# Optimization experiments

Measured on AMD Instinct MI355X. Metric: run time of the kernel, lower is better.

## Reference

```python
import jax, jax.numpy as jnp
import numpy as np

B = 16384          # graphs per batch
NUM_NODES = 32     # nodes per graph
EMBED = 64         # embed_dim (GCNConv in=out, conv1mult=1)
DEG = 8            # avg in-graph degree
OUT = 2            # outputSize
N = B * NUM_NODES
E = N * DEG
HID = NUM_NODES * EMBED  # size_in1 = size_out1 = 2048


def setup_inputs() -> dict:
    key = jax.random.key(0)
    ks = jax.random.split(key, 10)
    x = jax.random.normal(ks[0], (N, EMBED), dtype=jnp.float32)
    # edges constrained within each graph of NUM_NODES nodes
    offs = jnp.repeat(jnp.arange(B, dtype=jnp.int64) * NUM_NODES, DEG * NUM_NODES)
    src = jax.random.randint(ks[1], (E,), 0, NUM_NODES, dtype=jnp.int64) + offs
    dst = jax.random.randint(ks[2], (E,), 0, NUM_NODES, dtype=jnp.int64) + offs
    edge_index = jnp.stack([src, dst], axis=0)
    batch = jnp.repeat(jnp.arange(B, dtype=jnp.int64), NUM_NODES)
    s = 0.05
    Wc = jax.random.normal(ks[3], (EMBED, EMBED), dtype=jnp.float32) * s
    bc = jnp.zeros((EMBED,), dtype=jnp.float32)
    W1 = jax.random.normal(ks[4], (HID, HID), dtype=jnp.float32) * (1.0 / np.sqrt(HID))
    b1 = jnp.zeros((HID,), dtype=jnp.float32)
    W2 = jax.random.normal(ks[5], (OUT, HID), dtype=jnp.float32) * (1.0 / np.sqrt(HID))
    b2 = jnp.zeros((OUT,), dtype=jnp.float32)
    return {"x": x, "Wc": Wc, "bc": bc, "W1": W1, "b1": b1,
            "W2": W2, "b2": b2, "edge_index": edge_index, "batch": batch}


def gcn_conv(x, Wc, bc, edge_index):
    # PyG GCNConv: linear transform, add self-loops, symmetric normalization,
    # scatter-add aggregation at target nodes, then bias.
    n = x.shape[0]
    h = x @ Wc.T                                        # [N, F]
    loop = jnp.arange(n, dtype=edge_index.dtype)
    row = jnp.concatenate([edge_index[0], loop])        # sources
    col = jnp.concatenate([edge_index[1], loop])        # targets
    deg = jax.ops.segment_sum(jnp.ones_like(col, dtype=h.dtype), col,
                              num_segments=n)           # in-degree incl. self-loop
    dinv = jnp.where(deg > 0, jax.lax.rsqrt(deg), 0.0)
    norm = dinv[row] * dinv[col]                        # [E+N]
    msgs = h[row] * norm[:, None]                       # gather + scale
    out = jax.ops.segment_sum(msgs, col, num_segments=n)  # scatter-add
    return out + bc


def reference(x, Wc, bc, W1, b1, W2, b2, edge_index, batch):
    h = gcn_conv(x, Wc, bc, edge_index)
    h = jax.nn.relu(h)
    h = h.reshape(B, HID)                # [B, numNodes*embed_dim]
    h = h @ W1.T + b1                    # lin1 (dropout is eval-mode identity)
    h = jax.nn.relu(h)
    h = h @ W2.T + b2                    # lin2
    return jax.nn.softmax(h, axis=-1)    # [B, OUT]
```

## Files before the change

kernel.cpp:

```cpp
#include <hip/hip_runtime.h>

#define NGRAPH 16384
#define NNODE  32
#define EMB    64
#define HIDDIM 2048
#define ETOT   4194304
#define EPG    256

typedef __attribute__((ext_vector_type(8))) short bf16x8_t;
typedef __attribute__((ext_vector_type(8))) unsigned short u16x8_t;
typedef __attribute__((ext_vector_type(4))) float f32x4_t;

__device__ __forceinline__ unsigned short f2bf(float v) {
  unsigned int u = __float_as_uint(v);
  u += 0x7fffu + ((u >> 16) & 1u);
  return (unsigned short)(u >> 16);
}
__device__ __forceinline__ float bf2f(unsigned short u) {
  return __uint_as_float(((unsigned int)u) << 16);
}
__device__ __forceinline__ unsigned int cvtpk(float lo, float hi) {
  unsigned int r;
  asm("v_cvt_pk_bf16_f32 %0, %1, %2" : "=v"(r) : "v"(lo), "v"(hi));
  return r;
}
__device__ __forceinline__ bf16x8_t pack8(float4 a, float4 b) {
  union { unsigned int u[4]; bf16x8_t v; } r;
  r.u[0] = cvtpk(a.x, a.y); r.u[1] = cvtpk(a.z, a.w);
  r.u[2] = cvtpk(b.x, b.y); r.u[3] = cvtpk(b.z, b.w);
  return r.v;
}

#define GLDS(SRC, DST)                                                          \
  __builtin_amdgcn_global_load_lds(                                             \
      (const __attribute__((address_space(1))) void*)(SRC),                     \
      (__attribute__((address_space(3))) void*)(DST), 16, 0, 0)

__global__ __launch_bounds__(256, 4) void front_kernel(const float* __restrict__ x,
                                                       const float* __restrict__ Wc,
                                                       const float* __restrict__ bc,
                                                       const int* __restrict__ ei,
                                                       unsigned short* __restrict__ abf,
                                                       const float* __restrict__ W1,
                                                       unsigned short* __restrict__ W1b) {
  __shared__ __align__(16) char smem[40960];

  if (blockIdx.x >= 4096) {
    float* row = (float*)smem;
    const int r = blockIdx.x - 4096, t = threadIdx.x;
    const float4* p = (const float4*)(W1 + (size_t)r * HIDDIM);
    *(float4*)&row[t * 8]     = p[t * 2];
    *(float4*)&row[t * 8 + 4] = p[t * 2 + 1];
    __syncthreads();
    const int feat = t >> 2, nb = (t & 3) * 8;
    u16x8_t o;
    #pragma unroll
    for (int j = 0; j < 8; ++j) o[j] = f2bf(row[(nb + j) * 64 + feat]);
    *(u16x8_t*)(W1b + (size_t)r * HIDDIM + t * 8) = o;
    return;
  }

  const int wv = threadIdx.x >> 6, lane = threadIdx.x & 63;
  const int g = blockIdx.x * 4 + wv;
  char* my = smem + wv * 10240;
  unsigned int*   adjcnt = (unsigned int*)my;
  unsigned short* adjb   = (unsigned short*)my;
  unsigned short* outT   = (unsigned short*)my;
  unsigned short* hT     = (unsigned short*)(my + 5120);
  const int lr = lane & 15, lk = lane >> 4;

  const float* xg = x + (size_t)g * (NNODE * EMB);
  float4 xr[2][2][2];
  #pragma unroll
  for (int mt = 0; mt < 2; ++mt)
    #pragma unroll
    for (int kk = 0; kk < 2; ++kk) {
      const float* p = xg + (mt * 16 + lr) * EMB + kk * 32 + lk * 8;
      xr[mt][kk][0] = *(const float4*)p;
      xr[mt][kk][1] = *(const float4*)(p + 4);
    }

  int sl[4], dl[4];
  #pragma unroll
  for (int j = 0; j < 4; ++j) {
    sl[j] = ei[(size_t)g * EPG + j * 64 + lane] - g * NNODE;
    dl[j] = ei[(size_t)ETOT + (size_t)g * EPG + j * 64 + lane] - g * NNODE;
  }

  {
    uint4 z = {0u, 0u, 0u, 0u};
    #pragma unroll
    for (int i = 0; i < 4; ++i) *(uint4*)&adjcnt[lane * 16 + i * 4] = z;
  }
  asm volatile("" ::: "memory");
  #pragma unroll
  for (int j = 0; j < 4; ++j) atomicAdd(&adjcnt[dl[j] * 32 + sl[j]], 1u);
  asm volatile("" ::: "memory");

  const int rr = lane >> 1, hh = lane & 1;
  uint4 c[4];
  unsigned int cs = 0;
  #pragma unroll
  for (int i = 0; i < 4; ++i) {
    c[i] = *(const uint4*)&adjcnt[rr * 32 + hh * 16 + i * 4];
    cs += c[i].x + c[i].y + c[i].z + c[i].w;
  }
  cs += (unsigned int)__shfl_xor((int)cs, 1);
  const float dinvr = rsqrtf(1.0f + (float)cs);
  asm volatile("" ::: "memory");
  {
    float vals[16];
    #pragma unroll
    for (int i = 0; i < 4; ++i) {
      const unsigned int cc[4] = {c[i].x, c[i].y, c[i].z, c[i].w};
      #pragma unroll
      for (int e = 0; e < 4; ++e) {
        const int s = hh * 16 + i * 4 + e;
        const float ds = __shfl(dinvr, s * 2);
        const float cnt = (float)cc[e] + ((s == rr) ? 1.0f : 0.0f);
        vals[i * 4 + e] = cnt * dinvr * ds;
      }
    }
    union { unsigned int u[8]; u16x8_t v[2]; } pk;
    #pragma unroll
    for (int i = 0; i < 8; ++i) pk.u[i] = cvtpk(vals[2 * i], vals[2 * i + 1]);
    *(u16x8_t*)&adjb[rr * 40 + hh * 16]     = pk.v[0];
    *(u16x8_t*)&adjb[rr * 40 + hh * 16 + 8] = pk.v[1];
  }

  bf16x8_t xa[2][2];
  #pragma unroll
  for (int mt = 0; mt < 2; ++mt)
    #pragma unroll
    for (int kk = 0; kk < 2; ++kk) xa[mt][kk] = pack8(xr[mt][kk][0], xr[mt][kk][1]);
  f32x4_t hc[2][4];
  #pragma unroll
  for (int mt = 0; mt < 2; ++mt)
    #pragma unroll
    for (int nt = 0; nt < 4; ++nt) hc[mt][nt] = (f32x4_t){0.f, 0.f, 0.f, 0.f};
  #pragma unroll
  for (int nt = 0; nt < 4; ++nt)
    #pragma unroll
    for (int kk = 0; kk < 2; ++kk) {
      const float* p = Wc + (nt * 16 + lr) * EMB + kk * 32 + lk * 8;
      const bf16x8_t wb = pack8(*(const float4*)p, *(const float4*)(p + 4));
      #pragma unroll
      for (int mt = 0; mt < 2; ++mt)
        hc[mt][nt] = __builtin_amdgcn_mfma_f32_16x16x32_bf16(xa[mt][kk], wb, hc[mt][nt], 0, 0, 0);
    }
  #pragma unroll
  for (int mt = 0; mt < 2; ++mt)
    #pragma unroll
    for (int nt = 0; nt < 4; ++nt) {
      uint2 pk;
      pk.x = cvtpk(hc[mt][nt][0], hc[mt][nt][1]);
      pk.y = cvtpk(hc[mt][nt][2], hc[mt][nt][3]);
      *(uint2*)&hT[(nt * 16 + lr) * 40 + mt * 16 + lk * 4] = pk;
    }
  asm volatile("" ::: "memory");

  bf16x8_t aj[2];
  #pragma unroll
  for (int mt = 0; mt < 2; ++mt)
    aj[mt] = *(const bf16x8_t*)&adjb[(mt * 16 + lr) * 40 + lk * 8];
  f32x4_t oc[2][4];
  #pragma unroll
  for (int mt = 0; mt < 2; ++mt)
    #pragma unroll
    for (int nt = 0; nt < 4; ++nt) oc[mt][nt] = (f32x4_t){0.f, 0.f, 0.f, 0.f};
  #pragma unroll
  for (int nt = 0; nt < 4; ++nt) {
    const bf16x8_t hb = *(const bf16x8_t*)&hT[(nt * 16 + lr) * 40 + lk * 8];
    #pragma unroll
    for (int mt = 0; mt < 2; ++mt)
      oc[mt][nt] = __builtin_amdgcn_mfma_f32_16x16x32_bf16(aj[mt], hb, oc[mt][nt], 0, 0, 0);
  }
  asm volatile("" ::: "memory");

  #pragma unroll
  for (int nt = 0; nt < 4; ++nt) {
    const float bcv = bc[nt * 16 + lr];
    #pragma unroll
    for (int mt = 0; mt < 2; ++mt) {
      float v0 = fmaxf(oc[mt][nt][0] + bcv, 0.0f);
      float v1 = fmaxf(oc[mt][nt][1] + bcv, 0.0f);
      float v2 = fmaxf(oc[mt][nt][2] + bcv, 0.0f);
      float v3 = fmaxf(oc[mt][nt][3] + bcv, 0.0f);
      uint2 pk;
      pk.x = cvtpk(v0, v1);
      pk.y = cvtpk(v2, v3);
      *(uint2*)&outT[(nt * 16 + lr) * 40 + mt * 16 + lk * 4] = pk;
    }
  }
  asm volatile("" ::: "memory");

  unsigned short* og = abf + (size_t)g * HIDDIM;
  #pragma unroll
  for (int j = 0; j < 4; ++j) {
    const int e = lane * 8 + j * 512;
    const int feat = e >> 5, nb = e & 31;
    *(u16x8_t*)(og + e) = *(const u16x8_t*)&outT[feat * 40 + nb];
  }
}

__global__ __launch_bounds__(512, 1) void lin1_kernel(const unsigned short* __restrict__ A,
                                                      const unsigned short* __restrict__ Bw,
                                                      const float* __restrict__ b1,
                                                      const float* __restrict__ W2,
                                                      float2* __restrict__ part) {
  __shared__ __align__(16) unsigned short sh[65536];

  const int bid = blockIdx.x;
  const int xcd = bid & 7;
  const int g = bid >> 3;
  const int bm = xcd * 8 + (g >> 3);
  const int bn = g & 7;

  const int tid = threadIdx.x;
  const int lane = tid & 63, w = tid >> 6;
  const int wm = w >> 2, wn = w & 3;
  const int lr = lane & 15, lk = lane >> 4;

  const int r0 = tid >> 3;
  const int kge = ((((tid & 7) * 16) ^ ((r0 & 7) << 4)) >> 1);
  const unsigned short* gA = A  + (size_t)(bm * 256 + r0) * HIDDIM + kge;
  const unsigned short* gB = Bw + (size_t)(bn * 256 + r0) * HIDDIM + kge;

  auto stage = [&](const unsigned short* gb, int d, int mat, int half, int tile) {
    const unsigned short* s = gb + (size_t)(half * 128) * HIDDIM + tile * 64;
    unsigned short* l = &sh[d * 32768 + mat * 16384 + half * 8192 + tid * 8];
    GLDS(s, l);
    GLDS(s + (size_t)64 * HIDDIM, l + 4096);
  };

  const int arow = wm * 8192 + lr * 64;
  const int brow = 16384 + (wn >> 1) * 8192 + ((wn & 1) * 64 + lr) * 64;
  int eoff[2];
  eoff[0] = (lk * 8) ^ ((lr & 7) << 3);
  eoff[1] = (32 + lk * 8) ^ ((lr & 7) << 3);

  f32x4_t acc[8][4];
  #pragma unroll
  for (int i = 0; i < 8; ++i)
    #pragma unroll
    for (int j = 0; j < 4; ++j) acc[i][j] = (f32x4_t){0.f, 0.f, 0.f, 0.f};

  stage(gA, 0, 0, 0, 0); stage(gA, 0, 0, 1, 0);
  stage(gB, 0, 1, 0, 0); stage(gB, 0, 1, 1, 0);
  stage(gB, 1, 1, 0, 1); stage(gB, 1, 1, 1, 1);
  asm volatile("s_waitcnt vmcnt(4)" ::: "memory");
  __builtin_amdgcn_sched_barrier(0);
  __builtin_amdgcn_s_barrier();

  bf16x8_t af[4][2], bv0[2][2], bv1[2][2];

  for (int it = 0; it < 16; ++it) {
    const int o = 2 * it + 1;
    const bool more = (it < 15);

    #pragma unroll
    for (int half = 0; half < 2; ++half) {
      const int dof = half * 32768;

      #pragma unroll
      for (int mi = 0; mi < 4; ++mi) {
        af[mi][0] = *(const bf16x8_t*)&sh[dof + arow + mi * 1024 + eoff[0]];
        af[mi][1] = *(const bf16x8_t*)&sh[dof + arow + mi * 1024 + eoff[1]];
      }
      #pragma unroll
      for (int ni = 0; ni < 2; ++ni) {
        bv0[ni][0] = *(const bf16x8_t*)&sh[dof + brow + ni * 1024 + eoff[0]];
        bv0[ni][1] = *(const bf16x8_t*)&sh[dof + brow + ni * 1024 + eoff[1]];
        bv1[ni][0] = *(const bf16x8_t*)&sh[dof + brow + (ni + 2) * 1024 + eoff[0]];
        bv1[ni][1] = *(const bf16x8_t*)&sh[dof + brow + (ni + 2) * 1024 + eoff[1]];
      }
      if (half == 0)      { stage(gA, 1, 0, 0, o);     stage(gA, 1, 0, 1, o); }
      else if (more)      { stage(gA, 0, 0, 0, o + 1); stage(gA, 0, 0, 1, o + 1); }
      asm volatile("s_waitcnt lgkmcnt(0)" ::: "memory");
      __builtin_amdgcn_sched_barrier(0);
      __builtin_amdgcn_s_barrier();
      __builtin_amdgcn_s_setprio(1);
      #pragma unroll
      for (int kk = 0; kk < 2; ++kk)
        #pragma unroll
        for (int mi = 0; mi < 4; ++mi)
          #pragma unroll
          for (int ni = 0; ni < 2; ++ni) {
            acc[mi][ni]     = __builtin_amdgcn_mfma_f32_16x16x32_bf16(af[mi][kk], bv0[ni][kk], acc[mi][ni], 0, 0, 0);
            acc[mi][ni + 2] = __builtin_amdgcn_mfma_f32_16x16x32_bf16(af[mi][kk], bv1[ni][kk], acc[mi][ni + 2], 0, 0, 0);
          }
      __builtin_amdgcn_s_setprio(0);

      #pragma unroll
      for (int mi = 0; mi < 4; ++mi) {
        af[mi][0] = *(const bf16x8_t*)&sh[dof + arow + (mi + 4) * 1024 + eoff[0]];
        af[mi][1] = *(const bf16x8_t*)&sh[dof + arow + (mi + 4) * 1024 + eoff[1]];
      }
      if (more) {
        const int tgt = (half == 0) ? (o + 1) : (o + 2);
        stage(gB, half, 1, 0, tgt);
        stage(gB, half, 1, 1, tgt);
      }
      asm volatile("s_waitcnt lgkmcnt(0)" ::: "memory");
      if (more) { asm volatile("s_waitcnt vmcnt(4)" ::: "memory"); }
      else      { asm volatile("s_waitcnt vmcnt(0)" ::: "memory"); }
      __builtin_amdgcn_sched_barrier(0);
      __builtin_amdgcn_s_barrier();
      __builtin_amdgcn_s_setprio(1);
      #pragma unroll
      for (int kk = 0; kk < 2; ++kk)
        #pragma unroll
        for (int mi = 0; mi < 4; ++mi)
          #pragma unroll
          for (int ni = 0; ni < 2; ++ni) {
            acc[mi + 4][ni]     = __builtin_amdgcn_mfma_f32_16x16x32_bf16(af[mi][kk], bv0[ni][kk], acc[mi + 4][ni], 0, 0, 0);
            acc[mi + 4][ni + 2] = __builtin_amdgcn_mfma_f32_16x16x32_bf16(af[mi][kk], bv1[ni][kk], acc[mi + 4][ni + 2], 0, 0, 0);
          }
      __builtin_amdgcn_s_setprio(0);
    }
  }

  const int ccol0 = bn * 256 + wn * 64 + lr;
  float b1v[4], w2a[4], w2b[4];
  #pragma unroll
  for (int ni = 0; ni < 4; ++ni) {
    b1v[ni] = b1[ccol0 + ni * 16];
    w2a[ni] = W2[ccol0 + ni * 16];
    w2b[ni] = W2[HIDDIM + ccol0 + ni * 16];
  }
  float2* pl = (float2*)sh;
  #pragma unroll
  for (int mi = 0; mi < 8; ++mi)
    #pragma unroll
    for (int r = 0; r < 4; ++r) {
      float s0 = 0.0f, s1 = 0.0f;
      #pragma unroll
      for (int ni = 0; ni < 4; ++ni) {
        const float v = fmaxf(acc[mi][ni][r] + b1v[ni], 0.0f);
        s0 = fmaf(v, w2a[ni], s0);
        s1 = fmaf(v, w2b[ni], s1);
      }
      #pragma unroll
      for (int off = 1; off < 16; off <<= 1) {
        s0 += __shfl_xor(s0, off);
        s1 += __shfl_xor(s1, off);
      }
      if (lr == 0) {
        const int rowLocal = wm * 128 + mi * 16 + lk * 4 + r;
        float2 v2; v2.x = s0; v2.y = s1;
        pl[rowLocal * 4 + wn] = v2;
      }
    }
  __syncthreads();
  if (tid < 256) {
    const float2 p0 = pl[tid * 4 + 0];
    const float2 p1 = pl[tid * 4 + 1];
    const float2 p2 = pl[tid * 4 + 2];
    const float2 p3 = pl[tid * 4 + 3];
    float2 o;
    o.x = (p0.x + p1.x) + (p2.x + p3.x);
    o.y = (p0.y + p1.y) + (p2.y + p3.y);
    part[(size_t)bn * NGRAPH + bm * 256 + tid] = o;
  }
}

__global__ __launch_bounds__(256) void softmax_kernel(const float2* __restrict__ part,
                                                      const float* __restrict__ b2,
                                                      float* __restrict__ out) {
  const int i = blockIdx.x * 256 + threadIdx.x;
  float s0 = 0.0f, s1 = 0.0f;
  #pragma unroll
  for (int bn = 0; bn < 8; ++bn) {
    const float2 p = part[(size_t)bn * NGRAPH + i];
    s0 += p.x; s1 += p.y;
  }
  const float l0 = s0 + b2[0];
  const float l1 = s1 + b2[1];
  const float mx = fmaxf(l0, l1);
  const float e0 = expf(l0 - mx);
  const float e1 = expf(l1 - mx);
  const float inv = 1.0f / (e0 + e1);
  float2 o;
  o.x = e0 * inv;
  o.y = e1 * inv;
  *((float2*)out + i) = o;
}

extern "C" void kernel_launch(void* const* d_in, const int* in_sizes, int n_in,
                              void* d_out, int out_size, void* d_ws, size_t ws_size,
                              hipStream_t stream) {
  const float* x  = (const float*)d_in[0];
  const float* Wc = (const float*)d_in[1];
  const float* bc = (const float*)d_in[2];
  const float* W1 = (const float*)d_in[3];
  const float* b1 = (const float*)d_in[4];
  const float* W2 = (const float*)d_in[5];
  const float* b2 = (const float*)d_in[6];
  const int* ei   = (const int*)d_in[7];

  unsigned short* Abf  = (unsigned short*)d_ws;
  unsigned short* W1bf = (unsigned short*)((char*)d_ws + (size_t)67108864);
  float2*         part = (float2*)((char*)d_ws + (size_t)75497472);

  front_kernel<<<dim3(6144), dim3(256), 0, stream>>>(x, Wc, bc, ei, Abf, W1, W1bf);
  lin1_kernel<<<dim3(512), dim3(512), 0, stream>>>(Abf, W1bf, b1, W2, part);
  softmax_kernel<<<dim3(64), dim3(256), 0, stream>>>(part, b2, (float*)d_out);
}
```

Baseline: 166.0 us.

## Restructure lin1 GEMM pipeline to one barrier per K-tile with triple-buffered B

```diff
diff --git a/kernel.cpp b/kernel.cpp
--- a/kernel.cpp
+++ b/kernel.cpp
@@ -208,7 +208,7 @@
                                                       const float* __restrict__ b1,
                                                       const float* __restrict__ W2,
                                                       float2* __restrict__ part) {
-  __shared__ __align__(16) unsigned short sh[65536];
+  __shared__ __align__(16) unsigned short sh[81920];
 
   const int bid = blockIdx.x;
   const int xcd = bid & 7;
@@ -226,15 +226,21 @@
   const unsigned short* gA = A  + (size_t)(bm * 256 + r0) * HIDDIM + kge;
   const unsigned short* gB = Bw + (size_t)(bn * 256 + r0) * HIDDIM + kge;
 
-  auto stage = [&](const unsigned short* gb, int d, int mat, int half, int tile) {
-    const unsigned short* s = gb + (size_t)(half * 128) * HIDDIM + tile * 64;
-    unsigned short* l = &sh[d * 32768 + mat * 16384 + half * 8192 + tid * 8];
+  auto stageA = [&](int d, int half, int tile) {
+    const unsigned short* s = gA + (size_t)(half * 128) * HIDDIM + tile * 64;
+    unsigned short* l = &sh[d * 16384 + half * 8192 + tid * 8];
     GLDS(s, l);
     GLDS(s + (size_t)64 * HIDDIM, l + 4096);
   };
+  auto stageB = [&](int cb, int half, int tile) {
+    const unsigned short* s = gB + (size_t)(half * 128) * HIDDIM + tile * 64;
+    unsigned short* l = &sh[32768 + cb * 16384 + half * 8192 + tid * 8];
+    GLDS(s, l);
+    GLDS(s + (size_t)64 * HIDDIM, l + 4096);
+  };
 
   const int arow = wm * 8192 + lr * 64;
-  const int brow = 16384 + (wn >> 1) * 8192 + ((wn & 1) * 64 + lr) * 64;
+  const int brow = (wn >> 1) * 8192 + ((wn & 1) * 64 + lr) * 64;
   int eoff[2];
   eoff[0] = (lk * 8) ^ ((lr & 7) << 3);
   eoff[1] = (32 + lk * 8) ^ ((lr & 7) << 3);
@@ -245,79 +251,58 @@
     #pragma unroll
     for (int j = 0; j < 4; ++j) acc[i][j] = (f32x4_t){0.f, 0.f, 0.f, 0.f};
 
-  stage(gA, 0, 0, 0, 0); stage(gA, 0, 0, 1, 0);
-  stage(gB, 0, 1, 0, 0); stage(gB, 0, 1, 1, 0);
-  stage(gB, 1, 1, 0, 1); stage(gB, 1, 1, 1, 1);
+  stageA(0, 0, 0); stageA(0, 1, 0);
+  stageB(0, 0, 0); stageB(0, 1, 0);
+  stageB(1, 0, 1); stageB(1, 1, 1);
   asm volatile("s_waitcnt vmcnt(4)" ::: "memory");
   __builtin_amdgcn_sched_barrier(0);
   __builtin_amdgcn_s_barrier();
 
-  bf16x8_t af[4][2], bv0[2][2], bv1[2][2];
-
-  for (int it = 0; it < 16; ++it) {
-    const int o = 2 * it + 1;
-    const bool more = (it < 15);
-
-    #pragma unroll
-    for (int half = 0; half < 2; ++half) {
-      const int dof = half * 32768;
-
-      #pragma unroll
-      for (int mi = 0; mi < 4; ++mi) {
-        af[mi][0] = *(const bf16x8_t*)&sh[dof + arow + mi * 1024 + eoff[0]];
-        af[mi][1] = *(const bf16x8_t*)&sh[dof + arow + mi * 1024 + eoff[1]];
-      }
-      #pragma unroll
-      for (int ni = 0; ni < 2; ++ni) {
-        bv0[ni][0] = *(const bf16x8_t*)&sh[dof + brow + ni * 1024 + eoff[0]];
-        bv0[ni][1] = *(const bf16x8_t*)&sh[dof + brow + ni * 1024 + eoff[1]];
-        bv1[ni][0] = *(const bf16x8_t*)&sh[dof + brow + (ni + 2) * 1024 + eoff[0]];
-        bv1[ni][1] = *(const bf16x8_t*)&sh[dof + brow + (ni + 2) * 1024 + eoff[1]];
-      }
-      if (half == 0)      { stage(gA, 1, 0, 0, o);     stage(gA, 1, 0, 1, o); }
-      else if (more)      { stage(gA, 0, 0, 0, o + 1); stage(gA, 0, 0, 1, o + 1); }
-      asm volatile("s_waitcnt lgkmcnt(0)" ::: "memory");
-      __builtin_amdgcn_sched_barrier(0);
-      __builtin_amdgcn_s_barrier();
-      __builtin_amdgcn_s_setprio(1);
-      #pragma unroll
-      for (int kk = 0; kk < 2; ++kk)
+  int cb = 0;
+  for (int t = 0; t < 32; ++t) {
+    const int abase = (t & 1) * 16384;
+    const int bbase = 32768 + cb * 16384;
+
+    bf16x8_t af[8][2], bv[4][2];
+    #pragma unroll
+    for (int mi = 0; mi < 8; ++mi) {
+      af[mi][0] = *(const bf16x8_t*)&sh[abase + arow + mi * 1024 + eoff[0]];
+      af[mi][1] = *(const bf16x8_t*)&sh[abase + arow + mi * 1024 + eoff[1]];
+    }
+    #pragma unroll
+    for (int ni = 0; ni < 4; ++ni) {
+      bv[ni][0] = *(const bf16x8_t*)&sh[bbase + brow + ni * 1024 + eoff[0]];
+      bv[ni][1] = *(const bf16x8_t*)&sh[bbase + brow + ni * 1024 + eoff[1]];
+    }
+
+    if (t < 31) {
+      const int dn = (t + 1) & 1;
+      stageA(dn, 0, t + 1);
+      stageA(dn, 1, t + 1);
+    }
+    if (t < 30) {
+      const int c2 = (cb >= 1) ? cb - 1 : 2;
+      stageB(c2, 0, t + 2);
+      stageB(c2, 1, t + 2);
+    }
+
+    asm volatile("s_waitcnt lgkmcnt(0)" ::: "memory");
+    if (t < 30) { asm volatile("s_waitcnt vmcnt(4)" ::: "memory"); }
+    else        { asm volatile("s_waitcnt vmcnt(0)" ::: "memory"); }
+    __builtin_amdgcn_sched_barrier(0);
+    __builtin_amdgcn_s_barrier();
+
+    __builtin_amdgcn_s_setprio(1);
+    #pragma unroll
+    for (int kk = 0; kk < 2; ++kk)
+      #pragma unroll
+      for (int mi = 0; mi < 8; ++mi)
         #pragma unroll
-        for (int mi = 0; mi < 4; ++mi)
-          #pragma unroll
-          for (int ni = 0; ni < 2; ++ni) {
-            acc[mi][ni]     = __builtin_amdgcn_mfma_f32_16x16x32_bf16(af[mi][kk], bv0[ni][kk], acc[mi][ni], 0, 0, 0);
-            acc[mi][ni + 2] = __builtin_amdgcn_mfma_f32_16x16x32_bf16(af[mi][kk], bv1[ni][kk], acc[mi][ni + 2], 0, 0, 0);
-          }
-      __builtin_amdgcn_s_setprio(0);
-
-      #pragma unroll
-      for (int mi = 0; mi < 4; ++mi) {
-        af[mi][0] = *(const bf16x8_t*)&sh[dof + arow + (mi + 4) * 1024 + eoff[0]];
-        af[mi][1] = *(const bf16x8_t*)&sh[dof + arow + (mi + 4) * 1024 + eoff[1]];
-      }
-      if (more) {
-        const int tgt = (half == 0) ? (o + 1) : (o + 2);
-        stage(gB, half, 1, 0, tgt);
-        stage(gB, half, 1, 1, tgt);
-      }
-      asm volatile("s_waitcnt lgkmcnt(0)" ::: "memory");
-      if (more) { asm volatile("s_waitcnt vmcnt(4)" ::: "memory"); }
-      else      { asm volatile("s_waitcnt vmcnt(0)" ::: "memory"); }
-      __builtin_amdgcn_sched_barrier(0);
-      __builtin_amdgcn_s_barrier();
-      __builtin_amdgcn_s_setprio(1);
-      #pragma unroll
-      for (int kk = 0; kk < 2; ++kk)
-        #pragma unroll
-        for (int mi = 0; mi < 4; ++mi)
-          #pragma unroll
-          for (int ni = 0; ni < 2; ++ni) {
-            acc[mi + 4][ni]     = __builtin_amdgcn_mfma_f32_16x16x32_bf16(af[mi][kk], bv0[ni][kk], acc[mi + 4][ni], 0, 0, 0);
-            acc[mi + 4][ni + 2] = __builtin_amdgcn_mfma_f32_16x16x32_bf16(af[mi][kk], bv1[ni][kk], acc[mi + 4][ni + 2], 0, 0, 0);
-          }
-      __builtin_amdgcn_s_setprio(0);
-    }
+        for (int ni = 0; ni < 4; ++ni)
+          acc[mi][ni] = __builtin_amdgcn_mfma_f32_16x16x32_bf16(af[mi][kk], bv[ni][kk], acc[mi][ni], 0, 0, 0);
+    __builtin_amdgcn_s_setprio(0);
+
+    cb = (cb == 2) ? 0 : cb + 1;
   }
 
   const int ccol0 = bn * 256 + wn * 64 + lr;
```

New measurement: 175.8 us. 1.06x slower.
